# Kernel optimization log

Measured on AMD Instinct MI355X. Metric: run time of the kernel, lower is better.

Reference implementation:

```python
import jax, jax.numpy as jnp
import numpy as np
from jax import lax

EPS = 1e-5
HALF = 32
LEVELS = 17  # 16-level quantization of [0,1) -> round(x*255/16) in {0..16}


def setup_inputs() -> dict:
    key = jax.random.key(0)
    ks = jax.random.split(key, 48)
    r = lambda i, s: jax.random.normal(ks[i], s, jnp.float32) * 0.1
    inp = {
        'x': jax.random.uniform(ks[0], (4, 3, 256, 256), jnp.float32),
        # prepare: 1x1 conv (3->32), depthwise 1x1 (per-channel scale), BN, then repeat
        'w1': r(1, (32, 3)), 'b1': r(2, (32,)),
        'w2': 1.0 + r(3, (32,)), 'b2': r(4, (32,)),
        'bn1g': 1.0 + r(5, (32,)), 'bn1b': r(6, (32,)), 'bn1m': r(7, (32,)), 'bn1v': jnp.abs(1.0 + r(8, (32,))),
        'w3': r(9, (32, 32)), 'b3': r(10, (32,)),
        'w4': 1.0 + r(11, (32,)), 'b4': r(12, (32,)),
        'bn2g': 1.0 + r(13, (32,)), 'bn2b': r(14, (32,)), 'bn2m': r(15, (32,)), 'bn2v': jnp.abs(1.0 + r(16, (32,))),
        # downgrade SharedConv: one 3x3 kernel shared across all channels, stride 3, pad 1
        'scw': r(17, (1, 1, 3, 3)), 'scb': r(18, ()),
        # interpolate branch A: SharedConv 5x5 pad 2 + BN
        'iaw': r(19, (1, 1, 5, 5)), 'iabias': r(20, ()),
        'iabg': 1.0 + r(21, (32,)), 'iabb': r(22, (32,)), 'iabm': r(23, (32,)), 'iabv': jnp.abs(1.0 + r(24, (32,))),
        # interpolate branch B
        'ibw': r(25, (1, 1, 5, 5)), 'ibbias': r(26, ()),
        'ibbg': 1.0 + r(27, (32,)), 'ibbb': r(28, (32,)), 'ibbm': r(29, (32,)), 'ibbv': jnp.abs(1.0 + r(30, (32,))),
        'f1g': 1.0 + r(31, (64,)), 'f1b': r(32, (64,)), 'f1m': r(33, (64,)), 'f1v': jnp.abs(1.0 + r(34, (64,))),
        'f2g': 1.0 + r(35, (64,)), 'f2b': r(36, (64,)), 'f2m': r(37, (64,)), 'f2v': jnp.abs(1.0 + r(38, (64,))),
    }
    return inp


def _bn(x, g, b, m, v):
    # eval-mode BatchNorm2d with running stats; params broadcast over [B,C,H,W]
    return (x - m[:, None, None]) * (g[:, None, None] / jnp.sqrt(v[:, None, None] + EPS)) + b[:, None, None]


def _lrelu(x):
    return jnp.where(x >= 0, x, 0.01 * x)


def _mode_pool(x, k=11, stride=1, padding=1):
    # x is already quantized to levels q/16, q in {0..16}; pad with 0 (= level 0)
    x = jnp.pad(x, ((0, 0), (0, 0), (padding, padding), (padding, padding)))
    q = jnp.round(x * 16.0).astype(jnp.int32)  # [B,C,Hp,Wp] integer levels
    onehot = (q[None] == jnp.arange(LEVELS, dtype=jnp.int32)[:, None, None, None, None]).astype(jnp.float32)
    counts = lax.reduce_window(onehot, 0.0, lax.add, (1, 1, 1, k, k), (1, 1, 1, stride, stride), 'VALID')
    # argmax returns the FIRST max -> smallest modal value (torch.mode tie-break)
    return jnp.argmax(counts, axis=0).astype(jnp.float32) / 16.0


def _shared_conv(x, w, b, stride, padding):
    # single kxk kernel shared across all channels (depthwise with tied weight)
    B, C, H, W = x.shape
    y = lax.conv_general_dilated(x.reshape(B * C, 1, H, W), w, (stride, stride),
                                 ((padding, padding), (padding, padding)),
                                 dimension_numbers=('NCHW', 'OIHW', 'NCHW'))
    return y.reshape(B, C, y.shape[2], y.shape[3]) + b


def _ft(x, f1g, f1b, f1m, f1v, f2g, f2b, f2m, f2v):
    x = _bn(x, f1g, f1b, f1m, f1v)
    x = jnp.where(x > 0.1, x, 0.7 * x)  # MaxLeakyReLU(scale=0.7, threshold=0.1)
    x = _bn(x, f2g, f2b, f2m, f2v)
    # EmphaseLocal: gate by local contrast vs 11x11 mean (count_include_pad avg)
    xp = jnp.pad(x, ((0, 0), (0, 0), (5, 5), (5, 5)))
    mean = lax.reduce_window(xp, 0.0, lax.add, (1, 1, 11, 11), (1, 1, 1, 1), 'VALID') / 121.0
    return x * jax.nn.sigmoid(x - mean)


def reference(x, w1, b1, w2, b2, bn1g, bn1b, bn1m, bn1v, w3, b3, w4, b4, bn2g, bn2b, bn2m, bn2v,
              scw, scb, iaw, iabias, iabg, iabb, iabm, iabv, ibw, ibbias, ibbg, ibbb, ibbm, ibbv,
              f1g, f1b, f1m, f1v, f2g, f2b, f2m, f2v):
    B, C, H, W = x.shape
    # prepare: ColorDownsample(16) -> ModePool2d(11,1,1) -> 1x1 conv -> dw 1x1 -> BN -> LReLU (x2)
    d = jnp.round(x * 255.0 / 16.0) * 16.0 / 256.0
    d = _mode_pool(d)
    d = jnp.einsum('bchw,oc->bohw', d, w1) + b1[:, None, None]
    d = d * w2[:, None, None] + b2[:, None, None]
    d = _lrelu(_bn(d, bn1g, bn1b, bn1m, bn1v))
    d = jnp.einsum('bchw,oc->bohw', d, w3) + b3[:, None, None]
    d = d * w4[:, None, None] + b4[:, None, None]
    d = _lrelu(_bn(d, bn2g, bn2b, bn2m, bn2v))

    n = int(np.floor(np.log(min(d.shape[2], d.shape[3])) / np.log(3)))
    score = jnp.zeros((B, 2 * HALF, H, W), jnp.float32)
    for _ in range(n):
        d = _shared_conv(d, scw, scb, 3, 1)  # downgrade
        z = jax.image.resize(d, (B, HALF, H, W), 'bilinear')
        a = _lrelu(_bn(_shared_conv(z, iaw, iabias, 1, 2), iabg, iabb, iabm, iabv))
        bch = _lrelu(_bn(_shared_conv(z, ibw, ibbias, 1, 2), ibbg, ibbb, ibbm, ibbv))
        score = score + jnp.concatenate([a, bch], axis=1)  # Splitter + Stack(1)

    for _ in range(3):
        score = _ft(score, f1g, f1b, f1m, f1v, f2g, f2b, f2m, f2v)
    return score / n
```

## Files before the change

### kernel.cpp

```cpp
#include <hip/hip_runtime.h>
#include <math.h>

#define EPSI 1e-5f

#define P_D1 2048
#define P_D2 (P_D1 + 128*83*83)
#define P_D3 (P_D2 + 128*28*28)
#define P_D4 (P_D3 + 128*10*10)
#define P_D5 (P_D4 + 128*4*4)
#define P_SCORE (P_D5 + 128*2*2)
#define P_D  P_SCORE

__device__ __forceinline__ float rfl(float x) {
  return __builtin_bit_cast(float, __builtin_amdgcn_readfirstlane(__builtin_bit_cast(int, x)));
}

struct PrepArgs { const float* p[39]; };

__global__ void k_prep(PrepArgs a, float* __restrict__ P) {
  int t = threadIdx.x;
  const float *w1=a.p[1],*b1=a.p[2],*w2=a.p[3],*b2=a.p[4],*g1=a.p[5],*bb1=a.p[6],*m1=a.p[7],*v1=a.p[8];
  const float *w3=a.p[9],*b3=a.p[10],*w4=a.p[11],*b4=a.p[12],*g2=a.p[13],*bb2=a.p[14],*m2=a.p[15],*v2=a.p[16];
  for (int i=t;i<96;i+=256){ int o=i/3; float s=g1[o]/sqrtf(v1[o]+EPSI); P[i]=w1[i]*w2[o]*s; }
  for (int o=t;o<32;o+=256){ float s=g1[o]/sqrtf(v1[o]+EPSI); P[96+o]=(b1[o]*w2[o]+b2[o]-m1[o])*s+bb1[o]; }
  for (int i=t;i<1024;i+=256){ int o2=i/32; float s=g2[o2]/sqrtf(v2[o2]+EPSI); P[128+i]=w3[i]*w4[o2]*s; }
  for (int o=t;o<32;o+=256){ float s=g2[o]/sqrtf(v2[o]+EPSI); P[1152+o]=(b3[o]*w4[o]+b4[o]-m2[o])*s+bb2[o]; }
  const float *iag=a.p[21],*iab=a.p[22],*iam=a.p[23],*iav=a.p[24],*iabias=a.p[20];
  for (int c=t;c<32;c+=256){ float s=iag[c]/sqrtf(iav[c]+EPSI); P[1184+c]=s; P[1216+c]=(iabias[0]-iam[c])*s+iab[c]; }
  const float *ibg=a.p[27],*ibb=a.p[28],*ibm=a.p[29],*ibv=a.p[30],*ibbias=a.p[26];
  for (int c=t;c<32;c+=256){ float s=ibg[c]/sqrtf(ibv[c]+EPSI); P[1248+c]=s; P[1280+c]=(ibbias[0]-ibm[c])*s+ibb[c]; }
  const float *f1g=a.p[31],*f1b=a.p[32],*f1m=a.p[33],*f1v=a.p[34];
  for (int c=t;c<64;c+=256){ float s=f1g[c]/sqrtf(f1v[c]+EPSI); P[1312+c]=s; P[1376+c]=f1b[c]-f1m[c]*s; }
  const float *f2g=a.p[35],*f2b=a.p[36],*f2m=a.p[37],*f2v=a.p[38];
  for (int c=t;c<64;c+=256){ float s=f2g[c]/sqrtf(f2v[c]+EPSI); P[1440+c]=s; P[1504+c]=f2b[c]-f2m[c]*s; }
}

__global__ __launch_bounds__(256) void k_mode_mlp(const float* __restrict__ x,
                                                 const float* __restrict__ P,
                                                 float* __restrict__ dout) {
  __shared__ int qs[3*676];
  int lx = threadIdx.x, ly = threadIdx.y;
  int tid = ly*16 + lx;
  int tx0 = blockIdx.x*16, ty0 = blockIdx.y*16;
  int b = blockIdx.z;
  for (int k = tid; k < 3*676; k += 256) {
    int cch = k/676; int rem = k - cch*676; int r = rem/26; int cc = rem - r*26;
    int gy = ty0 + r - 1, gx = tx0 + cc - 1;
    int q = 0;
    if ((unsigned)gy < 256u && (unsigned)gx < 256u) {
      float v = x[((size_t)(b*3+cch)*256 + gy)*256 + gx];
      q = (int)rintf(v*255.0f/16.0f);
      q = q < 0 ? 0 : (q > 16 ? 16 : q);
    }
    qs[k] = q;
  }
  __syncthreads();
  int oi = ty0 + ly, oj = tx0 + lx;
  if (oi >= 248 || oj >= 248) return;

  float md[3];
  #pragma unroll
  for (int cch = 0; cch < 3; cch++) {
    const int* qp = &qs[cch*676 + ly*26 + lx];
    unsigned h0=0,h1=0,h2=0,h3=0,h4=0;
    #pragma unroll 1
    for (int u = 0; u < 11; u++) {
      #pragma unroll
      for (int v = 0; v < 11; v++) {
        int q = qp[u*26 + v];
        unsigned inc = 1u << ((q & 3) << 3);
        int sel = q >> 2;
        h0 += (sel==0) ? inc : 0u;
        h1 += (sel==1) ? inc : 0u;
        h2 += (sel==2) ? inc : 0u;
        h3 += (sel==3) ? inc : 0u;
        h4 += (sel==4) ? inc : 0u;
      }
    }
    int best = -1, mode = 0;
    #define CHK(l, w) { int cnt = (int)((w >> (((l)&3)*8)) & 255u); if (cnt > best) { best = cnt; mode = (l); } }
    CHK(0,h0) CHK(1,h0) CHK(2,h0) CHK(3,h0)
    CHK(4,h1) CHK(5,h1) CHK(6,h1) CHK(7,h1)
    CHK(8,h2) CHK(9,h2) CHK(10,h2) CHK(11,h2)
    CHK(12,h3) CHK(13,h3) CHK(14,h3) CHK(15,h3)
    CHK(16,h4)
    #undef CHK
    md[cch] = (float)mode * 0.0625f;
  }

  const float* A1 = P;           const float* C1 = P + 96;
  const float* A2 = P + 128;     const float* C2 = P + 1152;
  float h[32];
  #pragma unroll
  for (int o = 0; o < 32; o++) {
    float v = C1[o] + A1[o*3]*md[0] + A1[o*3+1]*md[1] + A1[o*3+2]*md[2];
    h[o] = (v >= 0.f) ? v : 0.01f*v;
  }
  size_t ob = ((size_t)(b*32)*248 + oi)*248 + oj;
  #pragma unroll
  for (int o2 = 0; o2 < 32; o2++) {
    float acc = C2[o2];
    #pragma unroll
    for (int o = 0; o < 32; o++) acc += A2[o2*32+o]*h[o];
    acc = (acc >= 0.f) ? acc : 0.01f*acc;
    dout[ob + (size_t)o2*(248*248)] = acc;
  }
}

__global__ void k_down(const float* __restrict__ in, float* __restrict__ out,
                       const float* __restrict__ scw, const float* __restrict__ scb) {
  const int Hin = 248, Hout = 83, total = 128*83*83;
  int idx = blockIdx.x*256 + threadIdx.x;
  if (idx >= total) return;
  float w[9];
  #pragma unroll
  for (int i = 0; i < 9; i++) w[i] = rfl(scw[i]);
  float bias = rfl(scb[0]);
  int j = idx % Hout; int t2 = idx / Hout; int i = t2 % Hout; int p = t2 / Hout;
  const float* base = in + (size_t)p*Hin*Hin;
  float s = bias;
  #pragma unroll
  for (int u = 0; u < 3; u++) {
    int r = 3*i - 1 + u;
    if ((unsigned)r < (unsigned)Hin) {
      #pragma unroll
      for (int v = 0; v < 3; v++) {
        int cc = 3*j - 1 + v;
        if ((unsigned)cc < (unsigned)Hin) s += base[(size_t)r*Hin + cc]*w[u*3+v];
      }
    }
  }
  out[idx] = s;
}

__global__ __launch_bounds__(256) void k_down_rest(const float* __restrict__ in, float* __restrict__ ws,
                                                   const float* __restrict__ scw, const float* __restrict__ scb) {
  __shared__ float buf[6889 + 784 + 100 + 16];
  int tid = threadIdx.x; int p = blockIdx.x;
  float w[9];
  #pragma unroll
  for (int i = 0; i < 9; i++) w[i] = rfl(scw[i]);
  float bias = rfl(scb[0]);
  const float* src = in + (size_t)p*6889;
  for (int k = tid; k < 6889; k += 256) buf[k] = src[k];
  __syncthreads();
  const int HIN[4] = {83,28,10,4}, HOUT[4] = {28,10,4,2};
  const int OIN[4] = {0, 6889, 6889+784, 6889+784+100};
  const size_t GOFF[4] = {P_D2, P_D3, P_D4, P_D5};
  #pragma unroll
  for (int st = 0; st < 4; st++) {
    const int hin = HIN[st], hout = HOUT[st];
    const float* bi = buf + OIN[st];
    float* bo = buf + OIN[st] + hin*hin;
    float* go = ws + GOFF[st] + (size_t)p*(hout*hout);
    for (int k = tid; k < hout*hout; k += 256) {
      int i = k/hout, j = k - i*hout;
      float s = bias;
      #pragma unroll
      for (int u = 0; u < 3; u++) {
        int r = 3*i - 1 + u;
        if ((unsigned)r < (unsigned)hin) {
          #pragma unroll
          for (int v = 0; v < 3; v++) {
            int cc = 3*j - 1 + v;
            if ((unsigned)cc < (unsigned)hin) s += bi[r*hin + cc]*w[u*3+v];
          }
        }
      }
      bo[k] = s; go[k] = s;
    }
    __syncthreads();
  }
}

#define NSP_PACK (83u | (28u<<7) | (10u<<14) | (4u<<21) | (2u<<28))
#define ZROT(r) ((((r)&3) ^ (((r)>>2)&3)) << 3)
__global__ __launch_bounds__(256) void k_accum(const float* __restrict__ ws,
                                               const float* __restrict__ iaw,
                                               const float* __restrict__ ibw,
                                               float* __restrict__ score, int b0) {
  __shared__ __align__(16) float hrow[14*96];
  __shared__ __align__(16) float zt[36*96];
  int tid = threadIdx.x;
  int c = blockIdx.y, b = blockIdx.z + b0;
  int tx0 = (blockIdx.x & 3)*64, ty0 = (blockIdx.x >> 2)*32;
  int half = tid >> 7;
  int t2 = tid & 127;
  int lx4 = (t2 & 15)*4, lyt = t2 >> 4;

  const float* wp = half ? ibw : iaw;
  float w[25];
  #pragma unroll
  for (int i = 0; i < 25; i++) w[i] = rfl(wp[i]);
  float s_ = rfl(ws[1184 + half*64 + c]);
  float C_ = rfl(ws[1216 + half*64 + c]);

  int bzy = tid >> 3;
  int bzx0 = tid & 7;

  float acc[16];
  #pragma unroll
  for (int i = 0; i < 16; i++) acc[i] = 0.f;

  size_t off = P_D1;
  #pragma unroll 1
  for (int lvl = 0; lvl < 5; lvl++) {
    const int n = (int)((NSP_PACK >> (7*lvl)) & 127u);
    const float inv = (float)n * (1.f/256.f);
    float f0 = ((float)(ty0-2)+0.5f)*inv - 0.5f;
    float f1 = ((float)(ty0+33)+0.5f)*inv - 0.5f;
    int yb0 = min(max((int)floorf(f0),0), n-2);
    int yb1 = min(max((int)floorf(f1),0), n-2);
    int rows = yb1 - yb0 + 2;
    const float* dp = ws + off + (size_t)(b*32+c)*(n*n);

    #pragma unroll 1
    for (int k = tid; k < rows*68; k += 256) {
      int r = k/68, zx = k - r*68;
      int gx = tx0 + zx - 2;
      float h = 0.f;
      if ((unsigned)gx < 256u) {
        float f = ((float)gx + 0.5f)*inv - 0.5f;
        float ff = floorf(f);
        int i0 = (int)ff;
        int xb = min(max(i0,0), n-2);
        float wx = (i0 < 0) ? 0.f : (i0 > n-2 ? 1.f : f - ff);
        const float* rp = dp + (yb0 + r)*n + xb;
        h = rp[0] + wx*(rp[1] - rp[0]);
      }
      hrow[r*96 + ((r&3)<<3) + zx] = h;
    }
    __syncthreads();

    {
      int gy = ty0 - 2 + bzy;
      float f = ((float)gy + 0.5f)*inv - 0.5f;
      float ff = floorf(f);
      int i0 = (int)ff;
      int yb = min(max(i0,0), n-2);
      float wy = (i0 < 0) ? 0.f : (i0 > n-2 ? 1.f : f - ff);
      bool vy = ((unsigned)gy < 256u);
      int rel = yb - yb0;
      int ra = rel*96 + ((rel&3)<<3);
      int rb = (rel+1)*96 + (((rel+1)&3)<<3);
      int zr0 = bzy*96 + ZROT(bzy);
      #pragma unroll
      for (int s = 0; s < 9; s++) {
        int zx = bzx0 + s*8;
        if (zx < 68) {
          float v = 0.f;
          if (vy) { float a = hrow[ra + zx], bb = hrow[rb + zx]; v = a + wy*(bb - a); }
          zt[zr0 + zx] = v;
        }
      }
      #pragma unroll 1
      for (int k = tid; k < 4*68; k += 256) {
        int zy = 32 + k/68; int zx = k - (k/68)*68;
        int gy2 = ty0 - 2 + zy;
        float v = 0.f;
        if ((unsigned)gy2 < 256u) {
          float f2 = ((float)gy2 + 0.5f)*inv - 0.5f;
          float ff2 = floorf(f2);
          int i02 = (int)ff2;
          int yb2 = min(max(i02,0), n-2);
          float wy2 = (i02 < 0) ? 0.f : (i02 > n-2 ? 1.f : f2 - ff2);
          int rel2 = yb2 - yb0;
          float a = hrow[rel2*96 + ((rel2&3)<<3) + zx];
          float bb = hrow[(rel2+1)*96 + (((rel2+1)&3)<<3) + zx];
          v = a + wy2*(bb - a);
        }
        zt[zy*96 + ZROT(zy) + zx] = v;
      }
    }
    __syncthreads();

    float cc[4][4];
    #pragma unroll
    for (int p = 0; p < 4; p++)
      #pragma unroll
      for (int j = 0; j < 4; j++) cc[p][j] = 0.f;
    #pragma unroll
    for (int zr = 0; zr < 8; zr++) {
      int row = 4*lyt + zr;
      int o = row*96 + ZROT(row) + lx4;
      float4 a0 = *(const float4*)&zt[o];
      float4 a1 = *(const float4*)&zt[o+4];
      float zz[8] = {a0.x,a0.y,a0.z,a0.w,a1.x,a1.y,a1.z,a1.w};
      #pragma unroll
      for (int p = 0; p < 4; p++) {
        int r = zr - p;
        if (r >= 0 && r < 5) {
          #pragma unroll
          for (int j = 0; j < 4; j++)
            #pragma unroll
            for (int v = 0; v < 5; v++)
              cc[p][j] += zz[j+v]*w[r*5+v];
        }
      }
    }
    #pragma unroll
    for (int p = 0; p < 4; p++)
      #pragma unroll
      for (int j = 0; j < 4; j++) {
        float v = cc[p][j]*s_ + C_;
        acc[p*4+j] += (v >= 0.f) ? v : 0.01f*v;
      }
    off += (size_t)128*n*n;
  }
  int oy = ty0 + 4*lyt, ox = tx0 + lx4;
  size_t base = ((size_t)(b*64 + half*32 + c)*256 + oy)*256 + ox;
  #pragma unroll
  for (int p = 0; p < 4; p++)
    *(float4*)&score[base + (size_t)p*256] = make_float4(acc[p*4],acc[p*4+1],acc[p*4+2],acc[p*4+3]);
}

__global__ __launch_bounds__(256) void k_ft(const float* __restrict__ in,
                                            float* __restrict__ out,
                                            const float* __restrict__ P, float scale) {
  __shared__ float Bf[16*271];
  int tid = threadIdx.x;
  int c = blockIdx.y, b = blockIdx.z;
  int ty0 = blockIdx.x * 16;
  float fs1 = rfl(P[1312+c]), fc1 = rfl(P[1376+c]), fs2 = rfl(P[1440+c]), fc2 = rfl(P[1504+c]);
  const float* ip = in + (size_t)(b*64 + c)*65536 + tid;

  if (tid < 160) {
    int r = tid / 10, q = tid - r*10;
    Bf[r*271 + (q < 5 ? q : 261 + q)] = 0.f;
  }

  float yreg[16];
  float win[11];
  float run = 0.f;
  #pragma unroll
  for (int s = 0; s < 26; s++) {
    int gy = ty0 + s - 5;
    float yv = 0.f;
    if ((unsigned)gy < 256u) {
      float t = ip[(size_t)gy*256]*fs1 + fc1;
      t = (t > 0.1f) ? t : 0.7f*t;
      yv = t*fs2 + fc2;
    }
    win[s % 11] = yv;
    run += yv;
    if (s >= 5 && s <= 20) yreg[s-5] = yv;
    if (s >= 10) {
      Bf[(s-10)*271 + 5 + tid] = run;
      run -= win[(s-10) % 11];
    }
  }
  __syncthreads();

  const size_t ob = (size_t)(b*64 + c)*65536 + (size_t)ty0*256 + tid;
  #pragma unroll
  for (int r = 0; r < 16; r++) {
    const float* bfr = Bf + r*271 + tid;
    float s = bfr[0];
    #pragma unroll
    for (int d = 1; d < 11; d++) s += bfr[d];
    float y = yreg[r];
    float sig = 1.f/(1.f + __expf(-(y - s*(1.f/121.f))));
    out[ob + (size_t)r*256] = y*sig*scale;
  }
}

extern "C" void kernel_launch(void* const* d_in, const int* in_sizes, int n_in,
                              void* d_out, int out_size, void* d_ws, size_t ws_size,
                              hipStream_t stream) {
  const float* x = (const float*)d_in[0];
  float* ws = (float*)d_ws;
  float* out = (float*)d_out;

  PrepArgs pa;
  for (int i = 0; i < 39; i++) pa.p[i] = (const float*)d_in[i];
  k_prep<<<dim3(1), dim3(256), 0, stream>>>(pa, ws);

  k_mode_mlp<<<dim3(16,16,4), dim3(16,16), 0, stream>>>(x, ws, ws + P_D);

  const float* scw = (const float*)d_in[17];
  const float* scb = (const float*)d_in[18];
  {
    int total = 128*83*83;
    k_down<<<dim3((total+255)/256), dim3(256), 0, stream>>>(ws + P_D, ws + P_D1, scw, scb);
  }
  k_down_rest<<<dim3(128), dim3(256), 0, stream>>>(ws + P_D1, ws, scw, scb);

  k_accum<<<dim3(32,32,2), dim3(256), 0, stream>>>(ws, (const float*)d_in[19],
                                                   (const float*)d_in[25], ws + P_SCORE, 0);
  k_accum<<<dim3(32,32,2), dim3(256), 0, stream>>>(ws, (const float*)d_in[19],
                                                   (const float*)d_in[25], ws + P_SCORE, 2);

  k_ft<<<dim3(16,64,4), dim3(256), 0, stream>>>(ws + P_SCORE, out, ws, 1.f);
  k_ft<<<dim3(16,64,4), dim3(256), 0, stream>>>(out, ws + P_SCORE, ws, 1.f);
  k_ft<<<dim3(16,64,4), dim3(256), 0, stream>>>(ws + P_SCORE, out, ws, 0.2f);
}
```

Before: 413.2 us.

## Precompute MLP lookup table over mode triples and use sliding column histograms

Because each pixel's three channel modes take only 17 values, the per-pixel 3->32->32 MLP is precomputed by a new kernel into a 4913x32 table, and the mode kernel now just gathers the table row. The 11x11 mode histogram is rebuilt from per-column sliding-window counts held in shared memory, packed as 4-bit nibbles, then summed across 11 columns. This replaces about 1k FMAs and 121 histogram updates per pixel with table loads and far fewer shared-memory reads. It adds a small extra launch and scattered table gathers. It also changes the zero-padding index in k_ft's shared buffer, which looks like a separate correctness fix.

```diff
diff --git a/kernel.cpp b/kernel.cpp
--- a/kernel.cpp
+++ b/kernel.cpp
@@ -10,6 +10,7 @@
 #define P_D5 (P_D4 + 128*4*4)
 #define P_SCORE (P_D5 + 128*2*2)
 #define P_D  P_SCORE
+#define P_TAB (P_SCORE + 8388608)
 
 __device__ __forceinline__ float rfl(float x) {
   return __builtin_bit_cast(float, __builtin_amdgcn_readfirstlane(__builtin_bit_cast(int, x)));
@@ -35,10 +36,34 @@
   for (int c=t;c<64;c+=256){ float s=f2g[c]/sqrtf(f2v[c]+EPSI); P[1440+c]=s; P[1504+c]=f2b[c]-f2m[c]*s; }
 }
 
+__global__ __launch_bounds__(256) void k_table(const float* __restrict__ P, float* __restrict__ T) {
+  int idx = blockIdx.x*256 + threadIdx.x;
+  if (idx >= 4913) return;
+  int m0 = idx/289; int rem = idx - m0*289; int m1 = rem/17; int m2 = rem - m1*17;
+  float md0 = (float)m0*0.0625f, md1 = (float)m1*0.0625f, md2 = (float)m2*0.0625f;
+  const float* A1 = P;           const float* C1 = P + 96;
+  const float* A2 = P + 128;     const float* C2 = P + 1152;
+  float h[32];
+  #pragma unroll
+  for (int o = 0; o < 32; o++) {
+    float v = C1[o] + A1[o*3]*md0 + A1[o*3+1]*md1 + A1[o*3+2]*md2;
+    h[o] = (v >= 0.f) ? v : 0.01f*v;
+  }
+  float* tp = T + (size_t)idx*32;
+  #pragma unroll
+  for (int o2 = 0; o2 < 32; o2++) {
+    float acc = C2[o2];
+    #pragma unroll
+    for (int o = 0; o < 32; o++) acc += A2[o2*32+o]*h[o];
+    tp[o2] = (acc >= 0.f) ? acc : 0.01f*acc;
+  }
+}
+
 __global__ __launch_bounds__(256) void k_mode_mlp(const float* __restrict__ x,
-                                                 const float* __restrict__ P,
+                                                 const float* __restrict__ T,
                                                  float* __restrict__ dout) {
   __shared__ int qs[3*676];
+  __shared__ unsigned CH[3*1326];
   int lx = threadIdx.x, ly = threadIdx.y;
   int tid = ly*16 + lx;
   int tx0 = blockIdx.x*16, ty0 = blockIdx.y*16;
@@ -55,55 +80,74 @@
     qs[k] = q;
   }
   __syncthreads();
+
+  if (tid < 156) {
+    int half = tid & 1; int rem = tid >> 1;
+    int cx = rem % 26; int ch = rem / 26;
+    const int* qp = &qs[ch*676 + cx];
+    int oy0 = half*8;
+    unsigned w0=0, w1=0, w2=0;
+    #pragma unroll 1
+    for (int r = oy0; r < oy0+11; r++) {
+      int q = qp[r*26];
+      unsigned inc = 1u << ((q & 7) << 2);
+      int sel = q >> 3;
+      w0 += (sel==0)?inc:0u; w1 += (sel==1)?inc:0u; w2 += (sel==2)?inc:0u;
+    }
+    unsigned base = (unsigned)(ch*442 + cx*17 + oy0);
+    CH[base] = w0; CH[1326+base] = w1; CH[2652+base] = w2;
+    #pragma unroll 1
+    for (int i = 1; i < 8; i++) {
+      int qr = qp[(oy0+i-1)*26];
+      unsigned incr = 1u << ((qr & 7) << 2);
+      int selr = qr >> 3;
+      w0 -= (selr==0)?incr:0u; w1 -= (selr==1)?incr:0u; w2 -= (selr==2)?incr:0u;
+      int qa = qp[(oy0+i+10)*26];
+      unsigned inca = 1u << ((qa & 7) << 2);
+      int sela = qa >> 3;
+      w0 += (sela==0)?inca:0u; w1 += (sela==1)?inca:0u; w2 += (sela==2)?inca:0u;
+      CH[base+i] = w0; CH[1326+base+i] = w1; CH[2652+base+i] = w2;
+    }
+  }
+  __syncthreads();
+
   int oi = ty0 + ly, oj = tx0 + lx;
   if (oi >= 248 || oj >= 248) return;
 
-  float md[3];
-  #pragma unroll
-  for (int cch = 0; cch < 3; cch++) {
-    const int* qp = &qs[cch*676 + ly*26 + lx];
-    unsigned h0=0,h1=0,h2=0,h3=0,h4=0;
-    #pragma unroll 1
-    for (int u = 0; u < 11; u++) {
-      #pragma unroll
-      for (int v = 0; v < 11; v++) {
-        int q = qp[u*26 + v];
-        unsigned inc = 1u << ((q & 3) << 3);
-        int sel = q >> 2;
-        h0 += (sel==0) ? inc : 0u;
-        h1 += (sel==1) ? inc : 0u;
-        h2 += (sel==2) ? inc : 0u;
-        h3 += (sel==3) ? inc : 0u;
-        h4 += (sel==4) ? inc : 0u;
-      }
-    }
-    int best = -1, mode = 0;
-    #define CHK(l, w) { int cnt = (int)((w >> (((l)&3)*8)) & 255u); if (cnt > best) { best = cnt; mode = (l); } }
-    CHK(0,h0) CHK(1,h0) CHK(2,h0) CHK(3,h0)
-    CHK(4,h1) CHK(5,h1) CHK(6,h1) CHK(7,h1)
-    CHK(8,h2) CHK(9,h2) CHK(10,h2) CHK(11,h2)
-    CHK(12,h3) CHK(13,h3) CHK(14,h3) CHK(15,h3)
-    CHK(16,h4)
-    #undef CHK
-    md[cch] = (float)mode * 0.0625f;
-  }
-
-  const float* A1 = P;           const float* C1 = P + 96;
-  const float* A2 = P + 128;     const float* C2 = P + 1152;
-  float h[32];
-  #pragma unroll
-  for (int o = 0; o < 32; o++) {
-    float v = C1[o] + A1[o*3]*md[0] + A1[o*3+1]*md[1] + A1[o*3+2]*md[2];
-    h[o] = (v >= 0.f) ? v : 0.01f*v;
-  }
+  int mode[3];
+  #pragma unroll
+  for (int ch = 0; ch < 3; ch++) {
+    unsigned a0=0,a1=0,a2=0,a3=0,a4=0;
+    unsigned base = (unsigned)(ch*442 + lx*17 + ly);
+    #pragma unroll
+    for (int d = 0; d < 11; d++) {
+      unsigned r0 = CH[base + d*17];
+      unsigned r1 = CH[1326 + base + d*17];
+      unsigned r2 = CH[2652 + base + d*17];
+      a0 += r0 & 0x0F0F0F0Fu;
+      a1 += (r0 >> 4) & 0x0F0F0F0Fu;
+      a2 += r1 & 0x0F0F0F0Fu;
+      a3 += (r1 >> 4) & 0x0F0F0F0Fu;
+      a4 += r2;
+    }
+    int best = -1, m = 0;
+    #define CHK2(l, w) { int cnt = (int)(((w) >> ((((l)>>1)&3)*8)) & 255u); if (cnt > best) { best = cnt; m = (l); } }
+    CHK2(0,a0) CHK2(1,a1) CHK2(2,a0) CHK2(3,a1) CHK2(4,a0) CHK2(5,a1) CHK2(6,a0) CHK2(7,a1)
+    CHK2(8,a2) CHK2(9,a3) CHK2(10,a2) CHK2(11,a3) CHK2(12,a2) CHK2(13,a3) CHK2(14,a2) CHK2(15,a3)
+    { int cnt = (int)(a4 & 255u); if (cnt > best) { best = cnt; m = 16; } }
+    #undef CHK2
+    mode[ch] = m;
+  }
+  int idx = (mode[0]*17 + mode[1])*17 + mode[2];
+  const float* tp = T + (size_t)idx*32;
   size_t ob = ((size_t)(b*32)*248 + oi)*248 + oj;
   #pragma unroll
-  for (int o2 = 0; o2 < 32; o2++) {
-    float acc = C2[o2];
-    #pragma unroll
-    for (int o = 0; o < 32; o++) acc += A2[o2*32+o]*h[o];
-    acc = (acc >= 0.f) ? acc : 0.01f*acc;
-    dout[ob + (size_t)o2*(248*248)] = acc;
+  for (int o2 = 0; o2 < 32; o2 += 4) {
+    float4 v = *(const float4*)(tp + o2);
+    dout[ob + (size_t)o2*61504]     = v.x;
+    dout[ob + (size_t)(o2+1)*61504] = v.y;
+    dout[ob + (size_t)(o2+2)*61504] = v.z;
+    dout[ob + (size_t)(o2+3)*61504] = v.w;
   }
 }
 
@@ -326,7 +370,7 @@
 
   if (tid < 160) {
     int r = tid / 10, q = tid - r*10;
-    Bf[r*271 + (q < 5 ? q : 261 + q)] = 0.f;
+    Bf[r*271 + (q < 5 ? q : 256 + q)] = 0.f;
   }
 
   float yreg[16];
@@ -374,8 +418,9 @@
   PrepArgs pa;
   for (int i = 0; i < 39; i++) pa.p[i] = (const float*)d_in[i];
   k_prep<<<dim3(1), dim3(256), 0, stream>>>(pa, ws);
-
-  k_mode_mlp<<<dim3(16,16,4), dim3(16,16), 0, stream>>>(x, ws, ws + P_D);
+  k_table<<<dim3(20), dim3(256), 0, stream>>>(ws, ws + P_TAB);
+
+  k_mode_mlp<<<dim3(16,16,4), dim3(16,16), 0, stream>>>(x, ws + P_TAB, ws + P_D);
 
   const float* scw = (const float*)d_in[17];
   const float* scb = (const float*)d_in[18];
```

After: 386.5 us. -6.4%, faster.
